# Kernel tuning notes

Measured on AMD Instinct MI355X. Metric: run time of the kernel, lower is better.

## Reference

```python
import jax, jax.numpy as jnp
import numpy as np
from functools import partial

T, B, I, H = 512, 64, 512, 512


def setup_inputs() -> dict:
    key = jax.random.key(0)
    ks = jax.random.split(key, 4)
    std = 0.01
    x = jax.random.normal(ks[0], (T, B, I), dtype=jnp.float32)
    a0 = jnp.zeros((B, H), dtype=jnp.float32)
    # packed gate weights, gate order: [update(u), forget(f), output(o), candidate(c)]
    W = jax.random.normal(ks[1], (I, 4 * H), dtype=jnp.float32) * std
    U = jax.random.normal(ks[2], (H, 4 * H), dtype=jnp.float32) * std
    b = jax.random.normal(ks[3], (4 * H,), dtype=jnp.float32) * std
    return {"x": x, "a0": a0, "W": W, "U": U, "b": b}


def reference(x, a0, W, U, b):
    h = a0.shape[-1]
    # precompute input projections for all timesteps: [T, B, 4H]
    xW = jnp.einsum("tbi,ig->tbg", x, W) + b

    def step(a_tm1, xw_t):
        g = xw_t + a_tm1 @ U  # [B, 4H]
        gamma_u = jax.nn.sigmoid(g[..., 0 * h:1 * h])
        gamma_f = jax.nn.sigmoid(g[..., 1 * h:2 * h])
        gamma_o = jax.nn.sigmoid(g[..., 2 * h:3 * h])
        c_tilde = jnp.tanh(g[..., 3 * h:4 * h])
        # NOTE: faithful to source — forget gate multiplies previous HIDDEN state
        c_t = gamma_u * c_tilde + gamma_f * a_tm1
        a_t = gamma_o * jnp.tanh(c_t)
        return a_t, a_t

    _, hs = jax.lax.scan(step, a0, xW)
    return hs  # [T, B, H]
```

## Files before the change

kernel.cpp:

```cpp
#include <hip/hip_runtime.h>
#include <cstddef>
#include <cstdint>


#define T_STEPS 512
#define NB      64
#define HID     512
#define G4      2048
#define KDIM    512
#define BB      8
#define NSL     16
#define BLK_DW  (NSL * 256)
#define PAR_DW  (BB * BLK_DW)

typedef short bf16x8 __attribute__((ext_vector_type(8)));
typedef float f32x4  __attribute__((ext_vector_type(4)));
typedef unsigned int u32x4 __attribute__((ext_vector_type(4)));

__device__ __forceinline__ float bf2f(unsigned short s) {
    unsigned u = ((unsigned)s) << 16;
    float f; __builtin_memcpy(&f, &u, 4); return f;
}
__device__ __forceinline__ unsigned short f2bf(float f) {
    unsigned u; __builtin_memcpy(&u, &f, 4);
    u = (u + 0x7FFFu + ((u >> 16) & 1u)) >> 16;
    return (unsigned short)u;
}
__device__ __forceinline__ unsigned min4(u32x4 v) {
    unsigned a = v[0] < v[1] ? v[0] : v[1];
    unsigned b = v[2] < v[3] ? v[2] : v[3];
    return a < b ? a : b;
}

__global__ void cast_x_kernel(const float* __restrict__ x,
                              unsigned short* __restrict__ o,
                              unsigned* __restrict__ abq) {
    if (blockIdx.x < 256)
        abq[blockIdx.x * 256 + threadIdx.x] = 0u;
    size_t i = (size_t)blockIdx.x * blockDim.x + threadIdx.x;
    float4 v = ((const float4*)x)[i];
    ushort4 r;
    r.x = f2bf(v.x); r.y = f2bf(v.y); r.z = f2bf(v.z); r.w = f2bf(v.w);
    ((ushort4*)o)[i] = r;
}

__global__ void transpose_cast(const float* __restrict__ src,
                               unsigned short* __restrict__ dst) {
    __shared__ float tile[64][65];
    const int n0 = blockIdx.x * 64;
    const int k0 = blockIdx.y * 64;
    const int c  = threadIdx.x & 63;
    const int r0 = threadIdx.x >> 6;
    for (int p = 0; p < 16; ++p) {
        int r = p * 4 + r0;
        tile[r][c] = src[(size_t)(k0 + r) * G4 + n0 + c];
    }
    __syncthreads();
    for (int p = 0; p < 16; ++p) {
        int r = p * 4 + r0;
        dst[(size_t)(n0 + r) * KDIM + k0 + c] = f2bf(tile[c][r]);
    }
}

__global__ __launch_bounds__(256) void gemm_xw(
        const unsigned short* __restrict__ A,
        const unsigned short* __restrict__ Bt,
        const float* __restrict__ bias,
        unsigned short* __restrict__ C) {
    __shared__ unsigned short As[128][56];
    __shared__ unsigned short Bs[128][56];
    const int m0 = blockIdx.x * 128;
    const int n0 = blockIdx.y * 128;
    const int tid = threadIdx.x;
    const int lane = tid & 63, wave = tid >> 6;
    const int quad = lane >> 4, l16 = lane & 15;
    const int wm = (wave >> 1) * 64, wn = (wave & 1) * 64;
    f32x4 acc[4][4];
    for (int i = 0; i < 4; ++i)
        for (int j = 0; j < 4; ++j) acc[i][j] = (f32x4)0.0f;
    const int srow = tid >> 2, scol = (tid & 3) * 8;
    for (int k0 = 0; k0 < KDIM; k0 += 32) {
        __syncthreads();
        for (int p = 0; p < 2; ++p) {
            int row = p * 64 + srow;
            *(uint4*)&As[row][scol] =
                *(const uint4*)&A[(size_t)(m0 + row) * KDIM + k0 + scol];
            *(uint4*)&Bs[row][scol] =
                *(const uint4*)&Bt[(size_t)(n0 + row) * KDIM + k0 + scol];
        }
        __syncthreads();
        bf16x8 af[4], bf[4];
        for (int i = 0; i < 4; ++i)
            af[i] = *(const bf16x8*)&As[wm + i * 16 + l16][quad * 8];
        for (int j = 0; j < 4; ++j)
            bf[j] = *(const bf16x8*)&Bs[wn + j * 16 + l16][quad * 8];
        for (int i = 0; i < 4; ++i)
            for (int j = 0; j < 4; ++j)
                acc[i][j] = __builtin_amdgcn_mfma_f32_16x16x32_bf16(
                    af[i], bf[j], acc[i][j], 0, 0, 0);
    }
    for (int i = 0; i < 4; ++i)
        for (int j = 0; j < 4; ++j) {
            int col = n0 + wn + j * 16 + l16;
            int g   = col >> 9;
            int u   = col & 511;
            int js  = u >> 5, utl = u & 31;
            float bv = bias[col];
            for (int r = 0; r < 4; ++r) {
                int row = m0 + wm + i * 16 + quad * 4 + r;
                int t = row >> 6, b = row & 63;
                size_t off = ((((size_t)t * BB + (b >> 3)) * NSL + js) * 4 + g)
                                 * 256 + (b & 7) * 32 + utl;
                C[off] = f2bf(acc[i][j][r] + bv);
            }
        }
}

__global__ __launch_bounds__(256, 1) void lstm_rec(
        const unsigned short* __restrict__ xWp,
        const unsigned short* __restrict__ Ut,
        const float* __restrict__ a0,
        float* __restrict__ out,
        unsigned* __restrict__ abq) {
    __shared__ unsigned short a_lds[16][520];
    __shared__ float gbuf[4][8][36];
    const int wgid  = blockIdx.x;
    const int i_blk = wgid & 7;
    const int j_sl  = wgid >> 3;
    const int tid   = threadIdx.x;
    const int wave  = tid >> 6;
    const int lane  = tid & 63;
    const int quad  = lane >> 4, l16 = lane & 15;
    const int j0 = j_sl * 32;
    const int b0 = i_blk * 8;
    const int bt = tid >> 5;
    const int ut = tid & 31;

    for (int i = tid; i < 2080; i += 256)
        ((unsigned*)&a_lds[8][0])[i] = 0u;

    bf16x8 bq[2][16];
#pragma unroll
    for (int n = 0; n < 2; ++n) {
        const unsigned short* urow =
            Ut + (size_t)(wave * HID + j0 + n * 16 + l16) * KDIM + quad * 8;
#pragma unroll
        for (int s = 0; s < 16; ++s)
            bq[n][s] = *(const bf16x8*)(urow + s * 32);
    }

    float aown = a0[(size_t)(b0 + bt) * HID + j0 + ut];
    {
        unsigned* pp = &abq[(size_t)i_blk * BLK_DW + j_sl * 256 + tid];
        unsigned pv = (unsigned)f2bf(aown) | (1u << 16);
        __hip_atomic_store(pp, pv, __ATOMIC_RELAXED, __HIP_MEMORY_SCOPE_WORKGROUP);
        __hip_atomic_store(pp, pv, __ATOMIC_RELAXED, __HIP_MEMORY_SCOPE_AGENT);
    }

    unsigned short xsA[4], xsB[4];
    {
        const unsigned short* xp =
            xWp + ((size_t)i_blk * NSL + j_sl) * 1024;
#pragma unroll
        for (int w = 0; w < 4; ++w)
            xsA[w] = xp[w * 256 + tid];
    }

    bool fast = true;

#define LOADS(FLAG)                                                         \
    asm volatile(                                                           \
        "global_load_dwordx4 %0, %4, off " FLAG "\n\t"                      \
        "global_load_dwordx4 %1, %5, off " FLAG "\n\t"                      \
        "global_load_dwordx4 %2, %6, off " FLAG "\n\t"                      \
        "global_load_dwordx4 %3, %7, off " FLAG "\n\t"                      \
        "s_waitcnt vmcnt(0)"                                                \
        : "=&v"(d0), "=&v"(d1), "=&v"(d2), "=&v"(d3)                        \
        : "v"(pc), "v"(pc + 256), "v"(pc + 512), "v"(pc + 768)              \
        : "memory")

    auto step = [&](int t, unsigned short* xs, unsigned short* xsn) {
        const unsigned* srcblk =
            abq + (size_t)(t & 1) * PAR_DW + (size_t)i_blk * BLK_DW;
        const u32x4* pc = (const u32x4*)srcblk + tid;
        const unsigned w16 = (unsigned)(t + 1) << 16;
        u32x4 d0, d1, d2, d3;
        bool okf;
        int tries = 0;
        do {
            if (__builtin_expect(fast, 1)) { LOADS("sc0"); }
            else                           { LOADS("sc1"); }
            unsigned m01 = min4(d0) < min4(d1) ? min4(d0) : min4(d1);
            unsigned m23 = min4(d2) < min4(d3) ? min4(d2) : min4(d3);
            okf = ((m01 < m23 ? m01 : m23) >= w16);
            if (!okf && ++tries > 32) fast = false;
        } while (!okf);

        {
            int tn = (t + 1 < T_STEPS) ? t + 1 : t;
            const unsigned short* xp =
                xWp + (((size_t)tn * BB + i_blk) * NSL + j_sl) * 1024;
#pragma unroll
            for (int w = 0; w < 4; ++w)
                xsn[w] = xp[w * 256 + tid];
        }

#define SCAT(q, d)                                                          \
        {                                                                   \
            int dd = ((q) << 10) + tid * 4;                                 \
            int bb = (dd >> 5) & 7;                                         \
            int kg = ((dd >> 8) << 5) | (dd & 31);                          \
            unsigned lo = ((d)[0] & 0xffffu) | ((d)[1] << 16);              \
            unsigned hi = ((d)[2] & 0xffffu) | ((d)[3] << 16);              \
            uint2 pk; pk.x = lo; pk.y = hi;                                 \
            *(uint2*)&a_lds[bb][kg] = pk;                                   \
        }
        SCAT(0, d0) SCAT(1, d1) SCAT(2, d2) SCAT(3, d3)
#undef SCAT
        __syncthreads();

        f32x4 acc0a = (f32x4)0.0f, acc0b = (f32x4)0.0f;
        f32x4 acc1a = (f32x4)0.0f, acc1b = (f32x4)0.0f;
#pragma unroll
        for (int s = 0; s < 16; s += 2) {
            bf16x8 af0 = *(const bf16x8*)&a_lds[l16][(s + 0) * 32 + quad * 8];
            bf16x8 af1 = *(const bf16x8*)&a_lds[l16][(s + 1) * 32 + quad * 8];
            acc0a = __builtin_amdgcn_mfma_f32_16x16x32_bf16(af0, bq[0][s + 0], acc0a, 0, 0, 0);
            acc1a = __builtin_amdgcn_mfma_f32_16x16x32_bf16(af0, bq[1][s + 0], acc1a, 0, 0, 0);
            acc0b = __builtin_amdgcn_mfma_f32_16x16x32_bf16(af1, bq[0][s + 1], acc0b, 0, 0, 0);
            acc1b = __builtin_amdgcn_mfma_f32_16x16x32_bf16(af1, bq[1][s + 1], acc1b, 0, 0, 0);
        }
        if (quad < 2) {
#pragma unroll
            for (int r = 0; r < 4; ++r) {
                gbuf[wave][quad * 4 + r][l16]      = acc0a[r] + acc0b[r];
                gbuf[wave][quad * 4 + r][16 + l16] = acc1a[r] + acc1b[r];
            }
        }
        __syncthreads();

        {
            float gu = gbuf[0][bt][ut] + bf2f(xs[0]);
            float gf = gbuf[1][bt][ut] + bf2f(xs[1]);
            float go = gbuf[2][bt][ut] + bf2f(xs[2]);
            float gc = gbuf[3][bt][ut] + bf2f(xs[3]);
            float su = 1.f / (1.f + __expf(-gu));
            float sf = 1.f / (1.f + __expf(-gf));
            float so = 1.f / (1.f + __expf(-go));
            float e2 = __expf(2.f * gc);
            float tc = 1.f - 2.f / (e2 + 1.f);
            float cc = su * tc + sf * aown;
            float ec = __expf(2.f * cc);
            float th = 1.f - 2.f / (ec + 1.f);
            float a  = so * th;
            aown = a;
            unsigned* pp = &abq[(size_t)((t + 1) & 1) * PAR_DW +
                                (size_t)i_blk * BLK_DW + j_sl * 256 + tid];
            unsigned pv = (unsigned)f2bf(a) | ((unsigned)(t + 2) << 16);
            __hip_atomic_store(pp, pv, __ATOMIC_RELAXED, __HIP_MEMORY_SCOPE_WORKGROUP);
            __hip_atomic_store(pp, pv, __ATOMIC_RELAXED, __HIP_MEMORY_SCOPE_AGENT);
            out[((size_t)t * NB + b0 + bt) * HID + j0 + ut] = a;
        }
    };

    for (int t = 0; t < T_STEPS; t += 2) {
        step(t,     xsA, xsB);
        step(t + 1, xsB, xsA);
    }
#undef LOADS
}

extern "C" void kernel_launch(void* const* d_in, const int* in_sizes, int n_in,
                              void* d_out, int out_size, void* d_ws, size_t ws_size,
                              hipStream_t stream) {
    (void)in_sizes; (void)n_in; (void)out_size; (void)ws_size;
    const float* x    = (const float*)d_in[0];
    const float* a0   = (const float*)d_in[1];
    const float* W    = (const float*)d_in[2];
    const float* U    = (const float*)d_in[3];
    const float* bias = (const float*)d_in[4];
    float* out = (float*)d_out;

    char* ws = (char*)d_ws;
    unsigned short* xbf  = (unsigned short*)(ws);
    unsigned short* Wt   = (unsigned short*)(ws + 33554432);
    unsigned short* Ut   = (unsigned short*)(ws + 35651584);
    unsigned short* xWp  = (unsigned short*)(ws + 37748736);
    unsigned*       abq  = (unsigned*)(ws + 171966464);

    cast_x_kernel<<<16384, 256, 0, stream>>>(x, xbf, abq);
    transpose_cast<<<dim3(32, 8), 256, 0, stream>>>(W, Wt);
    transpose_cast<<<dim3(32, 8), 256, 0, stream>>>(U, Ut);
    gemm_xw<<<dim3(256, 16), 256, 0, stream>>>(xbf, Wt, bias, xWp);
    lstm_rec<<<BB * NSL, 256, 0, stream>>>(xWp, Ut, a0, out, abq);
}
```

Measured before the change: 1.334 ms.

## Prefetch next-step hidden-state exchange loads and write own slice locally

```diff
diff --git a/kernel.cpp b/kernel.cpp
--- a/kernel.cpp
+++ b/kernel.cpp
@@ -136,6 +136,12 @@
     const int bt = tid >> 5;
     const int ut = tid & 31;
 
+    const bool own_row = (tid >> 6) == (j_sl & 3);
+    const unsigned fm0 = (own_row && (j_sl >> 2) == 0) ? 0xFFFFFFFFu : 0u;
+    const unsigned fm1 = (own_row && (j_sl >> 2) == 1) ? 0xFFFFFFFFu : 0u;
+    const unsigned fm2 = (own_row && (j_sl >> 2) == 2) ? 0xFFFFFFFFu : 0u;
+    const unsigned fm3 = (own_row && (j_sl >> 2) == 3) ? 0xFFFFFFFFu : 0u;
+
     for (int i = tid; i < 2080; i += 256)
         ((unsigned*)&a_lds[8][0])[i] = 0u;
 
@@ -150,12 +156,7 @@
     }
 
     float aown = a0[(size_t)(b0 + bt) * HID + j0 + ut];
-    {
-        unsigned* pp = &abq[(size_t)i_blk * BLK_DW + j_sl * 256 + tid];
-        unsigned pv = (unsigned)f2bf(aown) | (1u << 16);
-        __hip_atomic_store(pp, pv, __ATOMIC_RELAXED, __HIP_MEMORY_SCOPE_WORKGROUP);
-        __hip_atomic_store(pp, pv, __ATOMIC_RELAXED, __HIP_MEMORY_SCOPE_AGENT);
-    }
+    a_lds[bt][j0 + ut] = f2bf(aown);
 
     unsigned short xsA[4], xsB[4];
     {
@@ -167,8 +168,21 @@
     }
 
     bool fast = true;
-
-#define LOADS(FLAG)                                                         \
+    u32x4 d0, d1, d2, d3;
+    const u32x4* pc_cur;
+
+#define ISSUE(FLAG)                                                         \
+    asm volatile(                                                           \
+        "global_load_dwordx4 %0, %4, off " FLAG "\n\t"                      \
+        "global_load_dwordx4 %1, %5, off " FLAG "\n\t"                      \
+        "global_load_dwordx4 %2, %6, off " FLAG "\n\t"                      \
+        "global_load_dwordx4 %3, %7, off " FLAG                             \
+        : "=&v"(d0), "=&v"(d1), "=&v"(d2), "=&v"(d3)                        \
+        : "v"(pc_cur), "v"(pc_cur + 256), "v"(pc_cur + 512),                \
+          "v"(pc_cur + 768)                                                 \
+        : "memory")
+
+#define RELOAD(FLAG)                                                        \
     asm volatile(                                                           \
         "global_load_dwordx4 %0, %4, off " FLAG "\n\t"                      \
         "global_load_dwordx4 %1, %5, off " FLAG "\n\t"                      \
@@ -176,25 +190,37 @@
         "global_load_dwordx4 %3, %7, off " FLAG "\n\t"                      \
         "s_waitcnt vmcnt(0)"                                                \
         : "=&v"(d0), "=&v"(d1), "=&v"(d2), "=&v"(d3)                        \
-        : "v"(pc), "v"(pc + 256), "v"(pc + 512), "v"(pc + 768)              \
+        : "v"(pc_cur), "v"(pc_cur + 256), "v"(pc_cur + 512),                \
+          "v"(pc_cur + 768)                                                 \
         : "memory")
 
+    pc_cur = (const u32x4*)(abq + (size_t)i_blk * BLK_DW) + tid;
+    ISSUE("sc0");
+    {
+        unsigned* pp = &abq[(size_t)i_blk * BLK_DW + j_sl * 256 + tid];
+        unsigned pv = (unsigned)f2bf(aown) | (1u << 16);
+        __hip_atomic_store(pp, pv, __ATOMIC_RELAXED, __HIP_MEMORY_SCOPE_WORKGROUP);
+        __hip_atomic_store(pp, pv, __ATOMIC_RELAXED, __HIP_MEMORY_SCOPE_AGENT);
+    }
+
     auto step = [&](int t, unsigned short* xs, unsigned short* xsn) {
-        const unsigned* srcblk =
-            abq + (size_t)(t & 1) * PAR_DW + (size_t)i_blk * BLK_DW;
-        const u32x4* pc = (const u32x4*)srcblk + tid;
+        asm volatile("s_waitcnt vmcnt(2)"
+                     : "+v"(d0), "+v"(d1), "+v"(d2), "+v"(d3) :: "memory");
         const unsigned w16 = (unsigned)(t + 1) << 16;
-        u32x4 d0, d1, d2, d3;
-        bool okf;
+        unsigned m0 = min4(d0) | fm0, m1 = min4(d1) | fm1;
+        unsigned m2 = min4(d2) | fm2, m3 = min4(d3) | fm3;
+        unsigned ma = m0 < m1 ? m0 : m1, mb = m2 < m3 ? m2 : m3;
+        bool ok = ((ma < mb ? ma : mb) >= w16);
         int tries = 0;
-        do {
-            if (__builtin_expect(fast, 1)) { LOADS("sc0"); }
-            else                           { LOADS("sc1"); }
-            unsigned m01 = min4(d0) < min4(d1) ? min4(d0) : min4(d1);
-            unsigned m23 = min4(d2) < min4(d3) ? min4(d2) : min4(d3);
-            okf = ((m01 < m23 ? m01 : m23) >= w16);
-            if (!okf && ++tries > 32) fast = false;
-        } while (!okf);
+        while (!ok) {
+            if (__builtin_expect(fast, 1)) { RELOAD("sc0"); }
+            else                           { RELOAD("sc1"); }
+            m0 = min4(d0) | fm0; m1 = min4(d1) | fm1;
+            m2 = min4(d2) | fm2; m3 = min4(d3) | fm3;
+            ma = m0 < m1 ? m0 : m1; mb = m2 < m3 ? m2 : m3;
+            ok = ((ma < mb ? ma : mb) >= w16);
+            if (!ok && ++tries > 32) fast = false;
+        }
 
         {
             int tn = (t + 1 < T_STEPS) ? t + 1 : t;
@@ -215,7 +241,10 @@
             uint2 pk; pk.x = lo; pk.y = hi;                                 \
             *(uint2*)&a_lds[bb][kg] = pk;                                   \
         }
-        SCAT(0, d0) SCAT(1, d1) SCAT(2, d2) SCAT(3, d3)
+        if (!fm0) SCAT(0, d0)
+        if (!fm1) SCAT(1, d1)
+        if (!fm2) SCAT(2, d2)
+        if (!fm3) SCAT(3, d3)
 #undef SCAT
         __syncthreads();
 
@@ -254,12 +283,18 @@
             float th = 1.f - 2.f / (ec + 1.f);
             float a  = so * th;
             aown = a;
+            a_lds[bt][j0 + ut] = f2bf(a);
+            pc_cur = (const u32x4*)(abq + (size_t)((t + 1) & 1) * PAR_DW +
+                                    (size_t)i_blk * BLK_DW) + tid;
+            if (__builtin_expect(fast, 1)) { ISSUE("sc0"); }
+            else                           { ISSUE("sc1"); }
             unsigned* pp = &abq[(size_t)((t + 1) & 1) * PAR_DW +
                                 (size_t)i_blk * BLK_DW + j_sl * 256 + tid];
             unsigned pv = (unsigned)f2bf(a) | ((unsigned)(t + 2) << 16);
             __hip_atomic_store(pp, pv, __ATOMIC_RELAXED, __HIP_MEMORY_SCOPE_WORKGROUP);
             __hip_atomic_store(pp, pv, __ATOMIC_RELAXED, __HIP_MEMORY_SCOPE_AGENT);
-            out[((size_t)t * NB + b0 + bt) * HID + j0 + ut] = a;
+            __builtin_nontemporal_store(
+                a, &out[((size_t)t * NB + b0 + bt) * HID + j0 + ut]);
         }
     };
 
@@ -267,7 +302,8 @@
         step(t,     xsA, xsB);
         step(t + 1, xsB, xsA);
     }
-#undef LOADS
+#undef ISSUE
+#undef RELOAD
 }
 
 extern "C" void kernel_launch(void* const* d_in, const int* in_sizes, int n_in,
```

Result: slower. 1.503 ms (+12.7%).
